# Kernel optimization log

Hardware: AMD Instinct MI355X
Metric: run time of the kernel (lower is better)

The kernel has to match this reference:

```python
import jax, jax.numpy as jnp
import numpy as np

N = 500_000      # nodes
E = 4_000_000    # edges (avg degree 8)
F_IN = 24        # n_input (includeHeading=False, coords=False)
H = 64           # n_hidden
K = 6            # K_block Chebyshev order
OUT = 6          # n_output
EPS = 1e-5       # BatchNorm eps


def setup_inputs() -> dict:
    key = jax.random.key(0)
    ks = jax.random.split(key, 8)
    x = jax.random.normal(ks[0], (N, F_IN), dtype=jnp.float32)
    edge_index = jax.random.randint(ks[1], (2, E), 0, N, dtype=jnp.int32)
    # ChebConv(24 -> 64, K=6): stacked per-order weights [K, F_IN, H] + bias
    W1 = jax.random.normal(ks[2], (K, F_IN, H), dtype=jnp.float32) * (1.0 / np.sqrt(F_IN))
    b1 = jnp.zeros((H,), dtype=jnp.float32)
    # BatchNorm1d(64) affine params
    gamma = jnp.ones((H,), dtype=jnp.float32)
    beta = jnp.zeros((H,), dtype=jnp.float32)
    # conv_mix ChebConv(64 -> 6, K=1)
    Wmix = jax.random.normal(ks[3], (1, H, OUT), dtype=jnp.float32) * (1.0 / np.sqrt(H))
    bmix = jnp.zeros((OUT,), dtype=jnp.float32)
    return {"x": x, "edge_index": edge_index, "W1": W1, "b1": b1,
            "gamma": gamma, "beta": beta, "Wmix": Wmix, "bmix": bmix}


def cheb_conv(x, edge_index, W, b):
    """PyG ChebConv with normalization='sym', lambda_max=2.
    L_hat = L - I = -D^{-1/2} A D^{-1/2} (zero diagonal).
    """
    Kk = W.shape[0]
    row, col = edge_index[0], edge_index[1]  # messages flow row -> col
    deg = jax.ops.segment_sum(jnp.ones((E,), x.dtype), col, num_segments=N)
    dis = jnp.where(deg > 0, jax.lax.rsqrt(jnp.maximum(deg, 1.0)), 0.0)
    norm = -(dis[row] * dis[col])  # [E]

    def prop(h):  # h: [N, F] -> L_hat @ h via gather-scale-scatter
        return jax.ops.segment_sum(norm[:, None] * h[row], col, num_segments=N)

    Tx0 = x
    out = Tx0 @ W[0]
    if Kk > 1:
        Tx1 = prop(Tx0)
        out = out + Tx1 @ W[1]
        for k in range(2, Kk):
            Tx2 = 2.0 * prop(Tx1) - Tx0
            out = out + Tx2 @ W[k]
            Tx0, Tx1 = Tx1, Tx2
    return out + b


def reference(x, edge_index, W1, b1, gamma, beta, Wmix, bmix):
    # Kipfblock: ChebConv -> BatchNorm1d (batch stats) -> ReLU
    h = cheb_conv(x, edge_index, W1, b1)            # [N, H]
    mean = jnp.mean(h, axis=0)
    var = jnp.mean(jnp.square(h - mean), axis=0)    # biased var, as torch BN training
    h = (h - mean) * jax.lax.rsqrt(var + EPS) * gamma + beta
    h = jax.nn.relu(h)
    # conv_mix: ChebConv K=1 reduces to a dense linear (T_0 = x only)
    y = h @ Wmix[0] + bmix                          # [N, OUT]
    # F.dropout is identity in eval mode
    return y
```

## Files before the change

kernel.cpp:

```cpp
#include <hip/hip_runtime.h>
#include <hip/hip_fp16.h>

#define NN 500000
#define NE 4000000
#define FI 24
#define FH 64
#define KC 6
#define FO 6
#define BN_EPS 1e-5f

#define SLOTS 32
#define RH 32
#define NMT (NN / 16)
#define PASS_GRID 1024

#define SHARDS 8
#define EPT 8
#define CHUNK (256 * EPT)
#define NCHUNK ((NE + CHUNK - 1) / CHUNK)

#define RMASK 0x7FFFFu

typedef _Float16 half8 __attribute__((ext_vector_type(8)));
typedef float f32x4 __attribute__((ext_vector_type(4)));
typedef int int4v __attribute__((ext_vector_type(4)));
union U4H8 { uint4 u; half8 h; };


__device__ __forceinline__ void acc8(float* a, float d, uint4 u) {
    const __half2* h2 = (const __half2*)&u;
    #pragma unroll
    for (int j = 0; j < 4; ++j) {
        float2 f = __half22float2(h2[j]);
        a[2 * j]     += d * f.x;
        a[2 * j + 1] += d * f.y;
    }
}

__device__ __forceinline__ uint4 pack8(const float* a) {
    uint4 u;
    __half2* h2 = (__half2*)&u;
    #pragma unroll
    for (int j = 0; j < 4; ++j) h2[j] = __floats2half2_rn(a[2 * j], a[2 * j + 1]);
    return u;
}


__global__ __launch_bounds__(256) void k_fill(
    const int* __restrict__ row, const int* __restrict__ col,
    int* __restrict__ cnt, int* __restrict__ csrcT) {
    const int shard = blockIdx.x & (SHARDS - 1);
    const int chunk = blockIdx.x / SHARDS;
    const int base = chunk * CHUNK;
    #pragma unroll
    for (int i = 0; i < EPT / 4; ++i) {
        int e0 = base + (i * 256 + threadIdx.x) * 4;
        if (e0 + 4 <= NE) {
            int4v c4 = __builtin_nontemporal_load((const int4v*)(col + e0));
            #pragma unroll
            for (int j = 0; j < 4; ++j) {
                int c = c4[j];
                if ((c & (SHARDS - 1)) == shard) {
                    int r = __builtin_nontemporal_load(row + e0 + j);
                    int pos = atomicAdd(&cnt[c], 1);
                    if (pos < SLOTS) csrcT[(size_t)pos * NN + c] = r;
                }
            }
        } else {
            for (int j = 0; j < 4; ++j) {
                int e = e0 + j;
                if (e < NE) {
                    int c = col[e];
                    if ((c & (SHARDS - 1)) == shard) {
                        int r = row[e];
                        int pos = atomicAdd(&cnt[c], 1);
                        if (pos < SLOTS) csrcT[(size_t)pos * NN + c] = r;
                    }
                }
            }
        }
    }
}

__global__ void k_dis(const int* __restrict__ cnt, float* __restrict__ dis) {
    int n = blockIdx.x * blockDim.x + threadIdx.x;
    if (n < NN) {
        int d = cnt[n];
        dis[n] = d > 0 ? rsqrtf((float)d) : 0.0f;
    }
}


__global__ __launch_bounds__(256) void k_pack(
    const int* __restrict__ cnt, unsigned int* __restrict__ csrcT) {
    int n = blockIdx.x * 256 + threadIdx.x;
    if (n >= NN) return;
    int deg = cnt[n];
    if (deg > SLOTS) deg = SLOTS;
    for (int s = 0; s < deg; ++s) {
        size_t idx = (size_t)s * NN + n;
        unsigned int r = csrcT[idx] & RMASK;
        int dg = cnt[r];
        if (dg > 8191) dg = 8191;
        csrcT[idx] = r | ((unsigned int)dg << 19);
    }
}


__global__ void k_xhalf(const float* __restrict__ x, __half* __restrict__ Th0) {
    int n = blockIdx.x * blockDim.x + threadIdx.x;
    if (n >= NN) return;
    const float* r = x + (size_t)n * FI;
    float v[24];
    #pragma unroll
    for (int i = 0; i < 6; ++i) {
        float4 f = ((const float4*)r)[i];
        v[4 * i] = f.x; v[4 * i + 1] = f.y; v[4 * i + 2] = f.z; v[4 * i + 3] = f.w;
    }
    uint4* o = (uint4*)(Th0 + (size_t)n * RH);
    o[0] = pack8(v); o[1] = pack8(v + 8); o[2] = pack8(v + 16);
    o[3] = make_uint4(0, 0, 0, 0);
}


template<bool FIRST>
__global__ __launch_bounds__(256) void k_prop(
    const int* __restrict__ cnt, const unsigned int* __restrict__ csrcT,
    const float* __restrict__ dis,
    const __half* __restrict__ Tin, const __half* __restrict__ Tpp,
    __half* __restrict__ Tout) {
    int n = blockIdx.x * 256 + threadIdx.x;
    if (n >= NN) return;
    int deg = cnt[n];
    if (deg > SLOTS) deg = SLOTS;
    float a[24];
    #pragma unroll
    for (int j = 0; j < 24; ++j) a[j] = 0.0f;
    int s = 0;
    for (; s + 2 <= deg; s += 2) {
        unsigned int e0 = csrcT[(size_t)s * NN + n];
        unsigned int e1 = csrcT[(size_t)(s + 1) * NN + n];
        unsigned int r0 = e0 & RMASK, r1 = e1 & RMASK;
        unsigned int g0 = e0 >> 19,  g1 = e1 >> 19;
        float d0 = g0 ? rsqrtf((float)g0) : 0.0f;
        float d1 = g1 ? rsqrtf((float)g1) : 0.0f;
        const uint4* p0 = (const uint4*)(Tin + (size_t)r0 * RH);
        const uint4* p1 = (const uint4*)(Tin + (size_t)r1 * RH);
        uint4 u00 = p0[0], u01 = p0[1], u02 = p0[2];
        uint4 u10 = p1[0], u11 = p1[1], u12 = p1[2];
        acc8(a, d0, u00); acc8(a + 8, d0, u01); acc8(a + 16, d0, u02);
        acc8(a, d1, u10); acc8(a + 8, d1, u11); acc8(a + 16, d1, u12);
    }
    if (s < deg) {
        unsigned int e0 = csrcT[(size_t)s * NN + n];
        unsigned int r0 = e0 & RMASK;
        unsigned int g0 = e0 >> 19;
        float d0 = g0 ? rsqrtf((float)g0) : 0.0f;
        const uint4* p0 = (const uint4*)(Tin + (size_t)r0 * RH);
        acc8(a, d0, p0[0]); acc8(a + 8, d0, p0[1]); acc8(a + 16, d0, p0[2]);
    }
    float m = FIRST ? -dis[n] : -2.0f * dis[n];
    if (FIRST) {
        #pragma unroll
        for (int j = 0; j < 24; ++j) a[j] *= m;
    } else {
        const uint4* pr = (const uint4*)(Tpp + (size_t)n * RH);
        uint4 p0 = pr[0], p1 = pr[1], p2 = pr[2];
        float pv[24];
        {
            const __half2* h2 = (const __half2*)&p0;
            #pragma unroll
            for (int j = 0; j < 4; ++j) { float2 f = __half22float2(h2[j]); pv[2*j] = f.x; pv[2*j+1] = f.y; }
        }
        {
            const __half2* h2 = (const __half2*)&p1;
            #pragma unroll
            for (int j = 0; j < 4; ++j) { float2 f = __half22float2(h2[j]); pv[8+2*j] = f.x; pv[8+2*j+1] = f.y; }
        }
        {
            const __half2* h2 = (const __half2*)&p2;
            #pragma unroll
            for (int j = 0; j < 4; ++j) { float2 f = __half22float2(h2[j]); pv[16+2*j] = f.x; pv[16+2*j+1] = f.y; }
        }
        #pragma unroll
        for (int j = 0; j < 24; ++j) a[j] = m * a[j] - pv[j];
    }
    uint4* o = (uint4*)(Tout + (size_t)n * RH);
    o[0] = pack8(a); o[1] = pack8(a + 8); o[2] = pack8(a + 16);
    o[3] = make_uint4(0, 0, 0, 0);
}


__device__ __forceinline__ void build_bfrags(const float* __restrict__ W1, uint4* Bf) {
    for (int s = threadIdx.x; s < KC * 4 * 64; s += 256) {
        int lane = s & 63, blk = s >> 6;
        int seg = blk >> 2, nb = blk & 3;
        int q = lane >> 4, n = lane & 15;
        float v[8];
        #pragma unroll
        for (int j = 0; j < 8; ++j) {
            int k = q * 8 + j;
            v[j] = (k < FI) ? W1[(seg * FI + k) * FH + nb * 16 + n] : 0.0f;
        }
        U4H8 u;
        __half2* h2 = (__half2*)&u;
        #pragma unroll
        for (int j = 0; j < 4; ++j) h2[j] = __floats2half2_rn(v[2 * j], v[2 * j + 1]);
        Bf[s] = u.u;
    }
}

__global__ __launch_bounds__(256) void k_pass1(
    const __half* __restrict__ Th, const float* __restrict__ W1,
    const float* __restrict__ b1, float* __restrict__ stats,
    __half* __restrict__ h) {
    __shared__ uint4 Bf[KC * 4 * 64];
    __shared__ float st[2 * FH];
    build_bfrags(W1, Bf);
    if (threadIdx.x < 2 * FH) st[threadIdx.x] = 0.0f;
    __syncthreads();
    const int lane = threadIdx.x & 63;
    const int q = lane >> 4, ln = lane & 15;
    const int wid = blockIdx.x * 4 + (threadIdx.x >> 6);
    const int nw = gridDim.x * 4;
    float bias[4];
    #pragma unroll
    for (int nb = 0; nb < 4; ++nb) bias[nb] = b1[nb * 16 + ln];
    float ssum[4] = {0, 0, 0, 0}, sqsum[4] = {0, 0, 0, 0};
    for (int t = wid; t < NMT; t += nw) {
        const int n0 = t * 16;
        f32x4 acc[4];
        #pragma unroll
        for (int nb = 0; nb < 4; ++nb)
            acc[nb] = (f32x4){bias[nb], bias[nb], bias[nb], bias[nb]};
        #pragma unroll
        for (int seg = 0; seg < KC; ++seg) {
            U4H8 a;
            a.u = *(const uint4*)(Th + (size_t)seg * ((size_t)NN * RH)
                                  + (size_t)(n0 + ln) * RH + q * 8);
            #pragma unroll
            for (int nb = 0; nb < 4; ++nb) {
                U4H8 b; b.u = Bf[(seg * 4 + nb) * 64 + lane];
                acc[nb] = __builtin_amdgcn_mfma_f32_16x16x32_f16(a.h, b.h, acc[nb], 0, 0, 0);
            }
        }
        #pragma unroll
        for (int nb = 0; nb < 4; ++nb) {
            #pragma unroll
            for (int r = 0; r < 4; ++r) {
                float v = acc[nb][r];
                ssum[nb] += v;
                sqsum[nb] += v * v;
                h[(size_t)(n0 + q * 4 + r) * FH + nb * 16 + ln] = __float2half(v);
            }
        }
    }
    #pragma unroll
    for (int nb = 0; nb < 4; ++nb) {
        ssum[nb]  += __shfl_xor(ssum[nb], 16);  ssum[nb]  += __shfl_xor(ssum[nb], 32);
        sqsum[nb] += __shfl_xor(sqsum[nb], 16); sqsum[nb] += __shfl_xor(sqsum[nb], 32);
    }
    if (lane < 16) {
        #pragma unroll
        for (int nb = 0; nb < 4; ++nb) {
            atomicAdd(&st[nb * 16 + ln], ssum[nb]);
            atomicAdd(&st[FH + nb * 16 + ln], sqsum[nb]);
        }
    }
    __syncthreads();
    if (threadIdx.x < 2 * FH) atomicAdd(&stats[threadIdx.x], st[threadIdx.x]);
}

__global__ void k_finalize(const float* __restrict__ stats, const float* __restrict__ gamma,
                           const float* __restrict__ beta, float* __restrict__ ss) {
    int f = threadIdx.x;
    if (f < FH) {
        float mean = stats[f] * (1.0f / NN);
        float var  = stats[f + FH] * (1.0f / NN) - mean * mean;
        float rstd = rsqrtf(var + BN_EPS);
        float sc = gamma[f] * rstd;
        ss[f] = sc;
        ss[f + FH] = beta[f] - mean * sc;
    }
}


__global__ __launch_bounds__(256) void k_pass2(
    const __half* __restrict__ h, const float* __restrict__ ss,
    const float* __restrict__ Wmix, const float* __restrict__ bmix,
    float* __restrict__ y) {
    __shared__ float tab[FH * 8];
    for (int f = threadIdx.x; f < FH; f += 256) {
        tab[f * 8 + 0] = ss[f];
        tab[f * 8 + 1] = ss[FH + f];
        #pragma unroll
        for (int o = 0; o < FO; ++o) tab[f * 8 + 2 + o] = Wmix[f * FO + o];
    }
    __syncthreads();
    int n = blockIdx.x * 256 + threadIdx.x;
    if (n >= NN) return;
    const uint4* hr = (const uint4*)(h + (size_t)n * FH);
    float p[FO];
    #pragma unroll
    for (int o = 0; o < FO; ++o) p[o] = bmix[o];
    #pragma unroll
    for (int blk = 0; blk < 8; ++blk) {
        U4H8 u; u.u = hr[blk];
        const __half2* h2 = (const __half2*)&u;
        #pragma unroll
        for (int j = 0; j < 4; ++j) {
            float2 f2 = __half22float2(h2[j]);
            int f = blk * 8 + j * 2;
            {
                float4 t0 = *(const float4*)&tab[f * 8];
                float4 t1 = *(const float4*)&tab[f * 8 + 4];
                float hv = fmaxf(f2.x * t0.x + t0.y, 0.0f);
                p[0] += hv * t0.z; p[1] += hv * t0.w;
                p[2] += hv * t1.x; p[3] += hv * t1.y;
                p[4] += hv * t1.z; p[5] += hv * t1.w;
            }
            {
                float4 t0 = *(const float4*)&tab[(f + 1) * 8];
                float4 t1 = *(const float4*)&tab[(f + 1) * 8 + 4];
                float hv = fmaxf(f2.y * t0.x + t0.y, 0.0f);
                p[0] += hv * t0.z; p[1] += hv * t0.w;
                p[2] += hv * t1.x; p[3] += hv * t1.y;
                p[4] += hv * t1.z; p[5] += hv * t1.w;
            }
        }
    }
    float* yo = y + (size_t)n * FO;
    #pragma unroll
    for (int o = 0; o < FO; ++o) yo[o] = p[o];
}


extern "C" void kernel_launch(void* const* d_in, const int* in_sizes, int n_in,
                              void* d_out, int out_size, void* d_ws, size_t ws_size,
                              hipStream_t stream) {
    const float* x     = (const float*)d_in[0];
    const int*   edge  = (const int*)d_in[1];
    const float* W1    = (const float*)d_in[2];
    const float* b1    = (const float*)d_in[3];
    const float* gamma = (const float*)d_in[4];
    const float* beta  = (const float*)d_in[5];
    const float* Wmix  = (const float*)d_in[6];
    const float* bmix  = (const float*)d_in[7];
    float* y = (float*)d_out;

    const int* row = edge;
    const int* col = edge + NE;

    const size_t O_CNT   = 0;
    const size_t O_DIS   = 500000;
    const size_t O_STATS = 1000000;
    const size_t O_SS    = 1000128;
    const size_t O_CSRC  = 1000256;
    const size_t O_TH    = 17000256;
    const size_t TOTAL_ELEMS = O_TH + 6ull * NN * RH / 2;
    if (ws_size < TOTAL_ELEMS * 4ull) return;

    float* wf = (float*)d_ws;
    int*   wi = (int*)d_ws;
    int*   cnt   = wi + O_CNT;
    float* dis   = wf + O_DIS;
    float* stats = wf + O_STATS;
    float* ss    = wf + O_SS;
    int*   csrcT = wi + O_CSRC;
    __half* hbuf = (__half*)(wi + O_CSRC);
    __half* Th   = (__half*)(wf + O_TH);
    __half* Th0  = Th;
    __half* Th1  = Th + 1ull * NN * RH;
    __half* Th2  = Th + 2ull * NN * RH;
    __half* Th3  = Th + 3ull * NN * RH;
    __half* Th4  = Th + 4ull * NN * RH;
    __half* Th5  = Th + 5ull * NN * RH;

    (void)hipMemsetAsync(cnt,   0, NN * sizeof(int), stream);
    (void)hipMemsetAsync(stats, 0, 128 * sizeof(float), stream);

    const int BS = 256;
    const int GN = (NN + BS - 1) / BS;
    const int GF = NCHUNK * SHARDS;

    k_fill<<<GF, BS, 0, stream>>>(row, col, cnt, csrcT);
    k_dis<<<GN, BS, 0, stream>>>(cnt, dis);
    k_pack<<<GN, BS, 0, stream>>>(cnt, (unsigned int*)csrcT);
    k_xhalf<<<GN, BS, 0, stream>>>(x, Th0);

    k_prop<true ><<<GN, BS, 0, stream>>>(cnt, (const unsigned int*)csrcT, dis, Th0, nullptr, Th1);
    k_prop<false><<<GN, BS, 0, stream>>>(cnt, (const unsigned int*)csrcT, dis, Th1, Th0, Th2);
    k_prop<false><<<GN, BS, 0, stream>>>(cnt, (const unsigned int*)csrcT, dis, Th2, Th1, Th3);
    k_prop<false><<<GN, BS, 0, stream>>>(cnt, (const unsigned int*)csrcT, dis, Th3, Th2, Th4);
    k_prop<false><<<GN, BS, 0, stream>>>(cnt, (const unsigned int*)csrcT, dis, Th4, Th3, Th5);

    k_pass1<<<PASS_GRID, 256, 0, stream>>>(Th, W1, b1, stats, hbuf);
    k_finalize<<<1, 64, 0, stream>>>(stats, gamma, beta, ss);
    k_pass2<<<GN, 256, 0, stream>>>(hbuf, ss, Wmix, bmix, y);
}
```

Baseline: 881.8 us.

## Replace sharded atomic CSR fill with two-pass bucketed scatter and build

Edge-to-slot construction is split into two kernels. The first bins each edge chunk by destination bucket in shared memory and writes packed (row, local col) words contiguously into per-bucket buffers. The second builds each bucket's slot table using shared-memory atomics instead of global atomics on cnt. This removes the 8x redundant reads of col from the old sharded pass and the scattered global atomics, at the cost of an extra staging buffer (aliased onto Th5) and a fixed bucket capacity that could overflow on skewed inputs.

```diff
diff --git a/kernel.cpp b/kernel.cpp
--- a/kernel.cpp
+++ b/kernel.cpp
@@ -14,10 +14,13 @@
 #define NMT (NN / 16)
 #define PASS_GRID 1024
 
-#define SHARDS 8
 #define EPT 8
 #define CHUNK (256 * EPT)
 #define NCHUNK ((NE + CHUNK - 1) / CHUNK)
+
+#define BUCKETS 512
+#define BW 977
+#define BCAP 15500
 
 #define RMASK 0x7FFFFu
 
@@ -46,40 +49,88 @@
 }
 
 
-__global__ __launch_bounds__(256) void k_fill(
+__global__ __launch_bounds__(256) void k_scatter(
     const int* __restrict__ row, const int* __restrict__ col,
-    int* __restrict__ cnt, int* __restrict__ csrcT) {
-    const int shard = blockIdx.x & (SHARDS - 1);
-    const int chunk = blockIdx.x / SHARDS;
-    const int base = chunk * CHUNK;
+    unsigned int* __restrict__ ebuf, int* __restrict__ cur) {
+    __shared__ unsigned int val[CHUNK];
+    __shared__ unsigned short bk[CHUNK];
+    __shared__ int hist[BUCKETS], base[BUCKETS], rk[BUCKETS];
+    for (int t = threadIdx.x; t < BUCKETS; t += 256) { hist[t] = 0; rk[t] = 0; }
+    __syncthreads();
+    const int b0 = blockIdx.x * CHUNK;
     #pragma unroll
     for (int i = 0; i < EPT / 4; ++i) {
-        int e0 = base + (i * 256 + threadIdx.x) * 4;
+        int li4 = (i * 256 + threadIdx.x) * 4;
+        int e0 = b0 + li4;
         if (e0 + 4 <= NE) {
-            int4v c4 = __builtin_nontemporal_load((const int4v*)(col + e0));
+            int4v c4 = *(const int4v*)(col + e0);
+            int4v r4 = *(const int4v*)(row + e0);
             #pragma unroll
             for (int j = 0; j < 4; ++j) {
-                int c = c4[j];
-                if ((c & (SHARDS - 1)) == shard) {
-                    int r = __builtin_nontemporal_load(row + e0 + j);
-                    int pos = atomicAdd(&cnt[c], 1);
-                    if (pos < SLOTS) csrcT[(size_t)pos * NN + c] = r;
-                }
+                int c = c4[j], r = r4[j];
+                int b = c / BW, cl = c - b * BW;
+                val[li4 + j] = (unsigned int)r | ((unsigned int)cl << 19);
+                bk[li4 + j] = (unsigned short)b;
+                atomicAdd(&hist[b], 1);
             }
         } else {
             for (int j = 0; j < 4; ++j) {
-                int e = e0 + j;
+                int e = e0 + j, li = li4 + j;
                 if (e < NE) {
-                    int c = col[e];
-                    if ((c & (SHARDS - 1)) == shard) {
-                        int r = row[e];
-                        int pos = atomicAdd(&cnt[c], 1);
-                        if (pos < SLOTS) csrcT[(size_t)pos * NN + c] = r;
-                    }
+                    int c = col[e], r = row[e];
+                    int b = c / BW, cl = c - b * BW;
+                    val[li] = (unsigned int)r | ((unsigned int)cl << 19);
+                    bk[li] = (unsigned short)b;
+                    atomicAdd(&hist[b], 1);
+                } else {
+                    bk[li] = 0xFFFF;
                 }
             }
         }
     }
+    __syncthreads();
+    for (int t = threadIdx.x; t < BUCKETS; t += 256) {
+        int n = hist[t];
+        base[t] = n ? atomicAdd(&cur[t], n) : 0;
+    }
+    __syncthreads();
+    #pragma unroll
+    for (int i = 0; i < EPT / 4; ++i) {
+        int li4 = (i * 256 + threadIdx.x) * 4;
+        #pragma unroll
+        for (int j = 0; j < 4; ++j) {
+            int li = li4 + j;
+            int b = bk[li];
+            if (b != 0xFFFF) {
+                int rkk = atomicAdd(&rk[b], 1);
+                int pos = base[b] + rkk;
+                if (pos < BCAP) ebuf[(size_t)b * BCAP + pos] = val[li];
+            }
+        }
+    }
+}
+
+
+__global__ __launch_bounds__(256) void k_build(
+    const unsigned int* __restrict__ ebuf, const int* __restrict__ cur,
+    int* __restrict__ cnt, int* __restrict__ csrcT) {
+    __shared__ int cl_cnt[BW];
+    const int b = blockIdx.x;
+    const int nbase = b * BW;
+    const int width = (NN - nbase < BW) ? (NN - nbase) : BW;
+    for (int i = threadIdx.x; i < BW; i += 256) cl_cnt[i] = 0;
+    __syncthreads();
+    int nb = cur[b];
+    if (nb > BCAP) nb = BCAP;
+    for (int i = threadIdx.x; i < nb; i += 256) {
+        unsigned int v = ebuf[(size_t)b * BCAP + i];
+        int cl = v >> 19;
+        int r = v & RMASK;
+        int pos = atomicAdd(&cl_cnt[cl], 1);
+        if (pos < SLOTS) csrcT[(size_t)pos * NN + nbase + cl] = r;
+    }
+    __syncthreads();
+    for (int i = threadIdx.x; i < width; i += 256) cnt[nbase + i] = cl_cnt[i];
 }
 
 __global__ void k_dis(const int* __restrict__ cnt, float* __restrict__ dis) {
@@ -376,14 +427,17 @@
     __half* Th4  = Th + 4ull * NN * RH;
     __half* Th5  = Th + 5ull * NN * RH;
 
-    (void)hipMemsetAsync(cnt,   0, NN * sizeof(int), stream);
+    unsigned int* ebuf = (unsigned int*)Th5;
+    int* cur = (int*)(ebuf + (size_t)BUCKETS * BCAP);
+
+    (void)hipMemsetAsync(cur,   0, BUCKETS * sizeof(int), stream);
     (void)hipMemsetAsync(stats, 0, 128 * sizeof(float), stream);
 
     const int BS = 256;
     const int GN = (NN + BS - 1) / BS;
-    const int GF = NCHUNK * SHARDS;
-
-    k_fill<<<GF, BS, 0, stream>>>(row, col, cnt, csrcT);
+
+    k_scatter<<<NCHUNK, BS, 0, stream>>>(row, col, ebuf, cur);
+    k_build<<<BUCKETS, BS, 0, stream>>>(ebuf, cur, cnt, csrcT);
     k_dis<<<GN, BS, 0, stream>>>(cnt, dis);
     k_pack<<<GN, BS, 0, stream>>>(cnt, (unsigned int*)csrcT);
     k_xhalf<<<GN, BS, 0, stream>>>(x, Th0);
```

After: 765.5 us. 13.2% less time.
